# Performance work log

Measured on AMD Instinct MI355X. Metric: run time of the kernel, lower is better.

## Reference

```python
import jax, jax.numpy as jnp
import numpy as np

B, S, E = 16, 1024, 512
D = 2 * E            # dim of concatenated embeddings, input to QKV and MLP
H1, H2 = 2048, 1024  # hidden_dims
SCALE = float(1.0 / np.sqrt(E))  # code scales by embedding_dim**0.5 (the init arg, not D)


def setup_inputs() -> dict:
    key = jax.random.key(0)
    k = jax.random.split(key, 12)

    def lin_w(kk, fan_in, fan_out):
        return jax.random.normal(kk, (fan_in, fan_out), jnp.float32) * float(1.0 / np.sqrt(fan_in))

    return {
        "emb1": jax.random.normal(k[0], (B, S, E), jnp.float32),
        "emb2": jax.random.normal(k[1], (B, S, E), jnp.float32),
        # query-row masks; all ones (a 0 would -inf an entire softmax row -> NaN)
        "mask1": jnp.ones((B, S // 2), jnp.int32),
        "mask2": jnp.ones((B, S // 2), jnp.int32),
        "Wq": lin_w(k[2], D, D), "bq": jnp.zeros((D,), jnp.float32),
        "Wk": lin_w(k[3], D, D), "bk": jnp.zeros((D,), jnp.float32),
        "Wv": lin_w(k[4], D, D), "bv": jnp.zeros((D,), jnp.float32),
        "W1": lin_w(k[5], D, H1), "b1": jnp.zeros((H1,), jnp.float32),
        "W2": lin_w(k[6], H1, H2), "b2": jnp.zeros((H2,), jnp.float32),
        "W3": lin_w(k[7], H2, 1), "b3": jnp.zeros((1,), jnp.float32),
    }


def reference(emb1, emb2, mask1, mask2, Wq, bq, Wk, bk, Wv, bv, W1, b1, W2, b2, W3, b3):
    x = jnp.concatenate([emb1, emb2], axis=-1)        # [B, S, D]
    mask = jnp.concatenate([mask1, mask2], axis=-1)   # [B, S] (query-row mask)

    # QKV self-attention with query-only mask
    Q = x @ Wq + bq
    K = x @ Wk + bk
    V = x @ Wv + bv
    scores = jnp.einsum("bqd,bkd->bqk", Q, K) * SCALE  # [B, S, S]
    scores = jnp.where(mask[:, :, None] == 0, -jnp.inf, scores)
    attn = jax.nn.softmax(scores, axis=-1)
    attended = jnp.einsum("bqk,bkd->bqd", attn, V)     # [B, S, D]

    # MLP head (Dropout is identity in eval mode)
    h = jax.nn.relu(attended @ W1 + b1)
    h = jax.nn.relu(h @ W2 + b2)
    logits = h @ W3 + b3                               # [B, S, 1]
    return jax.nn.sigmoid(logits)
```

## Files before the change

### kernel.cpp

```cpp
#include <hip/hip_runtime.h>
#include <math.h>

#define DEV __device__ __forceinline__
#define SB0() __builtin_amdgcn_sched_barrier(0)

typedef unsigned short u16;
typedef unsigned int   u32;
typedef __bf16 bf16x8 __attribute__((ext_vector_type(8)));
typedef float  f32x4  __attribute__((ext_vector_type(4)));
typedef u16    u16x8  __attribute__((ext_vector_type(8)));
typedef u16    u16x4  __attribute__((ext_vector_type(4)));

DEV u16 f2b(float f) {
  u32 u = __builtin_bit_cast(u32, f);
  u = (u + 0x7FFFu + ((u >> 16) & 1u)) >> 16;
  return (u16)u;
}
DEV float b2f(u16 h) { u32 u = (u32)h << 16; return __builtin_bit_cast(float, u); }

DEV void gl_lds16(const u16* g, u16* l) {
  __builtin_amdgcn_global_load_lds((const __attribute__((address_space(1))) void*)g,
                                   (__attribute__((address_space(3))) void*)l, 16, 0, 0);
}

DEV float wred_max(float v) {
#pragma unroll
  for (int o = 32; o > 0; o >>= 1) v = fmaxf(v, __shfl_xor(v, o, 64));
  return v;
}
DEV float wred_sum(float v) {
#pragma unroll
  for (int o = 32; o > 0; o >>= 1) v += __shfl_xor(v, o, 64);
  return v;
}

__global__ __launch_bounds__(256) void prep(
    const float* __restrict__ e1, const float* __restrict__ e2, u16* __restrict__ xb,
    const float* __restrict__ Wq, const float* __restrict__ Wk, const float* __restrict__ Wv,
    const float* __restrict__ W1, const float* __restrict__ W2,
    u16* __restrict__ WTQKV, u16* __restrict__ W1T, u16* __restrict__ W2T,
    const float* __restrict__ bq, const float* __restrict__ bk, float* __restrict__ bf) {
  __shared__ float tile[64][65];
  const int bid = blockIdx.x;
  if (bid < 8192) {
    const size_t idx = ((size_t)bid * 256 + threadIdx.x) * 8;
    const int d = (int)(idx & 1023);
    const size_t row = idx >> 10;
    const float* s = (d < 512) ? (e1 + row * 512 + d) : (e2 + row * 512 + (d - 512));
    f32x4 a = *(const f32x4*)s;
    f32x4 b = *(const f32x4*)(s + 4);
    u16x8 o;
    o[0]=f2b(a[0]); o[1]=f2b(a[1]); o[2]=f2b(a[2]); o[3]=f2b(a[3]);
    o[4]=f2b(b[0]); o[5]=f2b(b[1]); o[6]=f2b(b[2]); o[7]=f2b(b[3]);
    *(u16x8*)(xb + idx) = o;
    return;
  }
  if (bid >= 9984) {
    int i = (bid - 9984) * 256 + threadIdx.x;
    bf[i] = (i < 1024) ? bq[i] : bk[i - 1024];
    return;
  }
  const float* W; u16* WT; int ldi, ldo, bx, by;
  if (bid < 8448)      { W = Wq; WT = WTQKV;              ldi = 1024; ldo = 1024; int v = bid - 8192; bx = v & 15; by = v >> 4; }
  else if (bid < 8704) { W = Wk; WT = WTQKV + 1024*1024;  ldi = 1024; ldo = 1024; int v = bid - 8448; bx = v & 15; by = v >> 4; }
  else if (bid < 8960) { W = Wv; WT = WTQKV + 2048*1024;  ldi = 1024; ldo = 1024; int v = bid - 8704; bx = v & 15; by = v >> 4; }
  else if (bid < 9472) { W = W1; WT = W1T;                ldi = 2048; ldo = 1024; int v = bid - 8960; bx = v & 31; by = v >> 5; }
  else                 { W = W2; WT = W2T;                ldi = 1024; ldo = 2048; int v = bid - 9472; bx = v & 15; by = v >> 4; }
  const int tx = threadIdx.x & 63, ty = threadIdx.x >> 6;
  const int r0 = by * 64, c0 = bx * 64;
#pragma unroll
  for (int i = 0; i < 16; ++i)
    tile[ty + 4*i][tx] = W[(size_t)(r0 + ty + 4*i) * ldi + c0 + tx];
  __syncthreads();
#pragma unroll
  for (int i = 0; i < 16; ++i)
    WT[(size_t)(c0 + ty + 4*i) * ldo + r0 + tx] = f2b(tile[tx][ty + 4*i]);
}

template<int F32OUT, int RELU, int RBIAS>
__global__ __launch_bounds__(512, 2) void gemm256(
    const u16* __restrict__ A, int lda, long long sA,
    const u16* __restrict__ B, int ldb, long long sB,
    void* __restrict__ C, int ldc, long long sC,
    const float* __restrict__ bias, float scale, int K) {
  __shared__ __align__(16) u16 lds[2][2][16384];

  const int t  = threadIdx.x;
  const int ln = t & 63, wv = t >> 6;

  int bx, by, bz;
  {
    const int gx = gridDim.x, gy = gridDim.y, gz = gridDim.z;
    const int nwg = gx * gy * gz;
    const int F = (blockIdx.z * gy + blockIdx.y) * gx + blockIdx.x;
    const int q = nwg >> 3;
    const int L = (F & 7) * q + (F >> 3);
    if (gz > 1) {
      const int pb = gx * gy;
      bz = L / pb; const int r = L - bz * pb;
      by = r / gx; bx = r - by * gx;
    } else {
      bz = 0;
      const int sh = ((gy & 7) == 0) ? 8 : 4;
      const int sw = gx * sh;
      const int sy = L / sw; const int r = L - sy * sw;
      bx = r / sh; by = sy * sh + (r - bx * sh);
    }
  }
  const int m0 = by * 256, n0 = bx * 256;
  A += (size_t)bz * (size_t)sA; B += (size_t)bz * (size_t)sB;

  const int gl = (ln & 7) ^ (ln >> 3);
  const u16* gAs = A + (size_t)(m0 + (t >> 3)) * lda + gl * 8;
  const u16* gBs = B + (size_t)(n0 + (t >> 3)) * ldb + gl * 8;

  const int l15 = ln & 15, lhi = ln >> 4;
  const int wm = (wv >> 2) * 128, wn = (wv & 3) * 64;
  const int colk0 = ((lhi ^ (l15 & 7)) << 3);
  const int colk1 = (((4 + lhi) ^ (l15 & 7)) << 3);
  const int rcA = (wv >> 2) * 8192 + l15 * 64;
  const int rcB = ((wv & 3) >> 1) * 8192 + (wv & 1) * 4096 + l15 * 64;

  f32x4 acc[8][4] = {};
  bf16x8 Af[4][2], Bf[4][2];
  const int KT = K >> 6, NIT = KT >> 1;

#define STG(T, OP, H, LD, GS)                                              \
  if ((T) < KT) {                                                          \
    const u16* _s = (GS) + (size_t)(H) * 128 * (size_t)(LD) + (size_t)(T) * 64; \
    u16* _d = &lds[(T) & 1][OP][(H) * 8192 + wv * 512];                    \
    gl_lds16(_s, _d); gl_lds16(_s + 64 * (size_t)(LD), _d + 4096);         \
  }
#define RDA(BUF, ILO) {                                                    \
  _Pragma("unroll") for (int ii = 0; ii < 4; ++ii) {                       \
    Af[ii][0] = *(const bf16x8*)&lds[BUF][0][rcA + ((ILO) + ii) * 1024 + colk0]; \
    Af[ii][1] = *(const bf16x8*)&lds[BUF][0][rcA + ((ILO) + ii) * 1024 + colk1]; } }
#define RDB(BUF, JLO) {                                                    \
  _Pragma("unroll") for (int jj = 0; jj < 2; ++jj) {                       \
    Bf[(JLO) + jj][0] = *(const bf16x8*)&lds[BUF][1][rcB + ((JLO) + jj) * 1024 + colk0]; \
    Bf[(JLO) + jj][1] = *(const bf16x8*)&lds[BUF][1][rcB + ((JLO) + jj) * 1024 + colk1]; } }
#define MM(ILO, JLO) {                                                     \
  _Pragma("unroll") for (int ii = 0; ii < 4; ++ii)                         \
  _Pragma("unroll") for (int jj = 0; jj < 2; ++jj) {                       \
    acc[(ILO)+ii][(JLO)+jj] = __builtin_amdgcn_mfma_f32_16x16x32_bf16(Af[ii][0], Bf[(JLO)+jj][0], acc[(ILO)+ii][(JLO)+jj], 0, 0, 0); \
    acc[(ILO)+ii][(JLO)+jj] = __builtin_amdgcn_mfma_f32_16x16x32_bf16(Af[ii][1], Bf[(JLO)+jj][1], acc[(ILO)+ii][(JLO)+jj], 0, 0, 0); } }
#define BAR() __builtin_amdgcn_s_barrier()
#define PRIO(x) __builtin_amdgcn_s_setprio(x)

  STG(0, 0, 0, lda, gAs); STG(0, 0, 1, lda, gAs);
  STG(0, 1, 0, ldb, gBs); STG(0, 1, 1, ldb, gBs);
  STG(1, 1, 0, ldb, gBs); STG(1, 1, 1, ldb, gBs);
  asm volatile("s_waitcnt vmcnt(4)" ::: "memory");
  SB0(); BAR();

  for (int it = 0; it < NIT; ++it) {
    const int T0 = it << 1, T1 = T0 + 1;
    RDB(0, 0); RDA(0, 0); STG(T1, 0, 0, lda, gAs);
    BAR();
    PRIO(1); MM(0, 0); PRIO(0); BAR();
    RDB(0, 2); STG(T1, 0, 1, lda, gAs);
    BAR();
    PRIO(1); MM(0, 2); PRIO(0); BAR();
    RDA(0, 4); STG(T0 + 2, 1, 0, ldb, gBs);
    BAR();
    PRIO(1); MM(4, 0); PRIO(0); BAR();
    STG(T0 + 2, 1, 1, ldb, gBs);
    BAR();
    PRIO(1); MM(4, 2); PRIO(0);
    if (T0 + 2 < KT) { asm volatile("s_waitcnt vmcnt(4)" ::: "memory"); }
    else             { asm volatile("s_waitcnt vmcnt(0)" ::: "memory"); }
    SB0(); BAR();
    RDB(1, 0); RDA(1, 0); STG(T0 + 2, 0, 0, lda, gAs);
    BAR();
    PRIO(1); MM(0, 0); PRIO(0); BAR();
    RDB(1, 2); STG(T0 + 2, 0, 1, lda, gAs);
    BAR();
    PRIO(1); MM(0, 2); PRIO(0); BAR();
    RDA(1, 4); STG(T0 + 3, 1, 0, ldb, gBs);
    BAR();
    PRIO(1); MM(4, 0); PRIO(0); BAR();
    STG(T0 + 3, 1, 1, ldb, gBs);
    BAR();
    PRIO(1); MM(4, 2); PRIO(0);
    if (T0 + 3 < KT) { asm volatile("s_waitcnt vmcnt(4)" ::: "memory"); }
    SB0(); BAR();
  }
#undef STG
#undef RDA
#undef RDB
#undef MM
#undef BAR
#undef PRIO

  const size_t cb = (size_t)bz * (size_t)sC;
  if (F32OUT) {
#pragma unroll
    for (int i = 0; i < 8; ++i) {
      const int rg = m0 + wm + i * 16 + lhi * 4;
#pragma unroll
      for (int j = 0; j < 4; ++j) {
        const int cg = n0 + wn + j * 16 + l15;
        const float cbv = (!RBIAS && bias) ? bias[cg] : 0.f;
#pragma unroll
        for (int r = 0; r < 4; ++r) {
          float v = acc[i][j][r] * scale + (RBIAS ? bias[rg + r] : cbv);
          if (RELU) v = fmaxf(v, 0.f);
          ((float*)C)[cb + (size_t)(rg + r) * ldc + cg] = v;
        }
      }
    }
  } else {
    u16* ep = ((u16*)lds) + wv * 8192;
#pragma unroll
    for (int i = 0; i < 8; ++i) {
      const int rg = m0 + wm + i * 16 + lhi * 4;
#pragma unroll
      for (int j = 0; j < 4; ++j) {
        const int cg = n0 + wn + j * 16 + l15;
        const float cbv = (!RBIAS && bias) ? bias[cg] : 0.f;
#pragma unroll
        for (int r = 0; r < 4; ++r) {
          float v = acc[i][j][r] * scale + (RBIAS ? bias[rg + r] : cbv);
          if (RELU) v = fmaxf(v, 0.f);
          const int lrow = i * 16 + lhi * 4 + r;
          const int lcol = (j * 16 + l15) ^ (((lrow >> 2) & 7) << 3);
          ep[lrow * 64 + lcol] = f2b(v);
        }
      }
    }
    asm volatile("s_waitcnt lgkmcnt(0)" ::: "memory");
    SB0();
    const int l3 = ln >> 3, c0 = (ln & 7) * 8;
#pragma unroll
    for (int rep = 0; rep < 16; ++rep) {
      const int lr = rep * 8 + l3;
      const int cs = c0 ^ (((lr >> 2) & 7) << 3);
      u16x8 v = *(const u16x8*)&ep[lr * 64 + cs];
      *(u16x8*)((u16*)C + cb + (size_t)(m0 + wm + lr) * ldc + n0 + wn + c0) = v;
    }
  }
}

__global__ __launch_bounds__(256) void softmax_mask(
    const float* __restrict__ sc, const int* __restrict__ m1,
    const int* __restrict__ m2, u16* __restrict__ attn) {
  __shared__ float red[8];
  const int row = blockIdx.x;
  const int b = row >> 10, q = row & 1023;
  const int mk = (q < 512) ? m1[b * 512 + q] : m2[b * 512 + q - 512];
  f32x4 v = ((const f32x4*)(sc + (size_t)row * 1024))[threadIdx.x];
  if (mk == 0) { v[0] = v[1] = v[2] = v[3] = -INFINITY; }
  float mx = fmaxf(fmaxf(v[0], v[1]), fmaxf(v[2], v[3]));
  mx = wred_max(mx);
  const int ln = threadIdx.x & 63, wv = threadIdx.x >> 6;
  if (ln == 0) red[wv] = mx;
  __syncthreads();
  mx = fmaxf(fmaxf(red[0], red[1]), fmaxf(red[2], red[3]));
  float e0 = __expf(v[0] - mx), e1 = __expf(v[1] - mx);
  float e2 = __expf(v[2] - mx), e3 = __expf(v[3] - mx);
  float s = wred_sum(e0 + e1 + e2 + e3);
  if (ln == 0) red[4 + wv] = s;
  __syncthreads();
  const float inv = 1.f / (red[4] + red[5] + red[6] + red[7]);
  u16x4 o; o[0] = f2b(e0 * inv); o[1] = f2b(e1 * inv); o[2] = f2b(e2 * inv); o[3] = f2b(e3 * inv);
  *(u16x4*)(attn + (size_t)row * 1024 + threadIdx.x * 4) = o;
}

__global__ __launch_bounds__(256) void logits_sigmoid(
    const u16* __restrict__ h2, const float* __restrict__ W3,
    const float* __restrict__ b3, float* __restrict__ out) {
  const int wid = (blockIdx.x * 256 + threadIdx.x) >> 6;
  const int ln = threadIdx.x & 63;
  const u16* r = h2 + (size_t)wid * 1024 + ln * 16;
  u16x8 v0 = *(const u16x8*)r;
  u16x8 v1 = *(const u16x8*)(r + 8);
  const float* w = W3 + ln * 16;
  float s = 0.f;
#pragma unroll
  for (int i = 0; i < 8; ++i) s += b2f(v0[i]) * w[i];
#pragma unroll
  for (int i = 0; i < 8; ++i) s += b2f(v1[i]) * w[8 + i];
#pragma unroll
  for (int o = 32; o > 0; o >>= 1) s += __shfl_down(s, o, 64);
  if (ln == 0) out[wid] = 1.f / (1.f + __expf(-(s + b3[0])));
}

extern "C" void kernel_launch(void* const* d_in, const int* in_sizes, int n_in,
                              void* d_out, int out_size, void* d_ws, size_t ws_size,
                              hipStream_t stream) {
  (void)in_sizes; (void)n_in; (void)out_size; (void)ws_size;
  const float* emb1 = (const float*)d_in[0];
  const float* emb2 = (const float*)d_in[1];
  const int*   mask1 = (const int*)d_in[2];
  const int*   mask2 = (const int*)d_in[3];
  const float* Wq = (const float*)d_in[4];  const float* bq = (const float*)d_in[5];
  const float* Wk = (const float*)d_in[6];  const float* bk = (const float*)d_in[7];
  const float* Wv = (const float*)d_in[8];  const float* bv = (const float*)d_in[9];
  const float* W1 = (const float*)d_in[10]; const float* b1 = (const float*)d_in[11];
  const float* W2 = (const float*)d_in[12]; const float* b2 = (const float*)d_in[13];
  const float* W3 = (const float*)d_in[14]; const float* b3 = (const float*)d_in[15];

  char* ws = (char*)d_ws;
  u16*  XB    = (u16*)(ws + 0);
  u16*  QK    = (u16*)(ws + 33554432);
  u16*  VT    = (u16*)(ws + 100663296);
  float* SC   = (float*)(ws + 134217728);
  u16*  WTQKV = (u16*)(ws + 201326592);
  u16*  W1T   = (u16*)(ws + 207618048);
  u16*  W2T   = (u16*)(ws + 211812352);
  float* BF_  = (float*)(ws + 216006656);
  u16*  ATTN  = XB;
  u16*  ATT   = (u16*)(ws + 134217728);
  u16*  H1    = QK;
  u16*  H2    = VT;
  float* out  = (float*)d_out;

  const float SCALE = 0.04419417382415922f;

  prep<<<9992, 256, 0, stream>>>(emb1, emb2, XB, Wq, Wk, Wv, W1, W2,
                                 WTQKV, W1T, W2T, bq, bk, BF_);

  gemm256<0, 0, 0><<<dim3(8, 64, 1), 512, 0, stream>>>(
      XB, 1024, 0, WTQKV, 1024, 0, QK, 2048, 0, BF_, 1.f, 1024);
  gemm256<0, 0, 1><<<dim3(64, 4, 1), 512, 0, stream>>>(
      WTQKV + 2048 * 1024, 1024, 0, XB, 1024, 0, VT, 16384, 0, bv, 1.f, 1024);
  gemm256<1, 0, 0><<<dim3(4, 4, 16), 512, 0, stream>>>(
      QK, 2048, 2097152LL, QK + 1024, 2048, 2097152LL,
      SC, 1024, 1048576LL, nullptr, SCALE, 1024);
  softmax_mask<<<16384, 256, 0, stream>>>(SC, mask1, mask2, ATTN);
  gemm256<0, 0, 0><<<dim3(4, 4, 16), 512, 0, stream>>>(
      ATTN, 1024, 1048576LL, VT, 16384, 1024LL,
      ATT, 1024, 1048576LL, nullptr, 1.f, 1024);
  gemm256<0, 1, 0><<<dim3(8, 64, 1), 512, 0, stream>>>(
      ATT, 1024, 0, W1T, 1024, 0, H1, 2048, 0, b1, 1.f, 1024);
  gemm256<0, 1, 0><<<dim3(4, 64, 1), 512, 0, stream>>>(
      H1, 2048, 0, W2T, 2048, 0, H2, 1024, 0, b2, 1.f, 2048);
  logits_sigmoid<<<4096, 256, 0, stream>>>(H2, W3, b3, out);
}
```

Baseline: 362.7 us.

## Fuse softmax into score GEMM epilogue and MLP head into last GEMM

The score GEMM now writes unnormalised bf16 exp values, with the mask applied, directly to the attention buffer, and accumulates row sums atomically. The PV GEMM divides by those row sums in its epilogue. This removes the fp32 score matrix round trip and the separate softmax kernel. The final W2 GEMM folds relu and the W3 dot product into its epilogue with atomic adds, replacing the H2 write and the logits kernel with a tiny sigmoid kernel. Exp is taken without subtracting the row max, so it can overflow if score magnitudes grow. Atomic accumulation also makes the row-sum order nondeterministic.

```diff
diff --git a/kernel.cpp b/kernel.cpp
--- a/kernel.cpp
+++ b/kernel.cpp
@@ -21,17 +21,6 @@
 DEV void gl_lds16(const u16* g, u16* l) {
   __builtin_amdgcn_global_load_lds((const __attribute__((address_space(1))) void*)g,
                                    (__attribute__((address_space(3))) void*)l, 16, 0, 0);
-}
-
-DEV float wred_max(float v) {
-#pragma unroll
-  for (int o = 32; o > 0; o >>= 1) v = fmaxf(v, __shfl_xor(v, o, 64));
-  return v;
-}
-DEV float wred_sum(float v) {
-#pragma unroll
-  for (int o = 32; o > 0; o >>= 1) v += __shfl_xor(v, o, 64);
-  return v;
 }
 
 __global__ __launch_bounds__(256) void prep(
@@ -77,12 +66,14 @@
     WT[(size_t)(c0 + ty + 4*i) * ldo + r0 + tx] = f2b(tile[tx][ty + 4*i]);
 }
 
-template<int F32OUT, int RELU, int RBIAS>
+template<int MODE>
 __global__ __launch_bounds__(512, 2) void gemm256(
     const u16* __restrict__ A, int lda, long long sA,
     const u16* __restrict__ B, int ldb, long long sB,
     void* __restrict__ C, int ldc, long long sC,
-    const float* __restrict__ bias, float scale, int K) {
+    const float* __restrict__ bias, float scale, int K,
+    const int* __restrict__ mk1, const int* __restrict__ mk2,
+    float* __restrict__ rsw, const float* __restrict__ w3, float* __restrict__ lg) {
   __shared__ __align__(16) u16 lds[2][2][16384];
 
   const int t  = threadIdx.x;
@@ -193,96 +184,99 @@
 #undef PRIO
 
   const size_t cb = (size_t)bz * (size_t)sC;
-  if (F32OUT) {
+
+  if (MODE == 5) {
+    float w3v[4];
+#pragma unroll
+    for (int j = 0; j < 4; ++j) w3v[j] = w3[n0 + wn + j * 16 + l15];
 #pragma unroll
     for (int i = 0; i < 8; ++i) {
       const int rg = m0 + wm + i * 16 + lhi * 4;
 #pragma unroll
-      for (int j = 0; j < 4; ++j) {
-        const int cg = n0 + wn + j * 16 + l15;
-        const float cbv = (!RBIAS && bias) ? bias[cg] : 0.f;
-#pragma unroll
-        for (int r = 0; r < 4; ++r) {
-          float v = acc[i][j][r] * scale + (RBIAS ? bias[rg + r] : cbv);
-          if (RELU) v = fmaxf(v, 0.f);
-          ((float*)C)[cb + (size_t)(rg + r) * ldc + cg] = v;
+      for (int r = 0; r < 4; ++r) {
+        float s = 0.f;
+#pragma unroll
+        for (int j = 0; j < 4; ++j) {
+          float v = acc[i][j][r] + bias[n0 + wn + j * 16 + l15];
+          v = fmaxf(v, 0.f);
+          s += v * w3v[j];
         }
+        s += __shfl_xor(s, 1, 64); s += __shfl_xor(s, 2, 64);
+        s += __shfl_xor(s, 4, 64); s += __shfl_xor(s, 8, 64);
+        if (l15 == 0) atomicAdd(&lg[rg + r], s);
+      }
+    }
+    return;
+  }
+
+  u16* ep = ((u16*)lds) + wv * 8192;
+
+  if (MODE == 3) {
+#pragma unroll
+    for (int i = 0; i < 8; ++i) {
+#pragma unroll
+      for (int r = 0; r < 4; ++r) {
+        const int rr = m0 + wm + i * 16 + lhi * 4 + r;
+        const int mk = (rr < 512) ? mk1[bz * 512 + rr] : mk2[bz * 512 + rr - 512];
+        const int lrow = i * 16 + lhi * 4 + r;
+        float s = 0.f;
+#pragma unroll
+        for (int j = 0; j < 4; ++j) {
+          float e = (mk != 0) ? __expf(acc[i][j][r] * scale) : 0.f;
+          const u16 eb = f2b(e);
+          s += b2f(eb);
+          const int lcol = (j * 16 + l15) ^ (((lrow >> 2) & 7) << 3);
+          ep[lrow * 64 + lcol] = eb;
+        }
+        s += __shfl_xor(s, 1, 64); s += __shfl_xor(s, 2, 64);
+        s += __shfl_xor(s, 4, 64); s += __shfl_xor(s, 8, 64);
+        if (l15 == 0) atomicAdd(&rsw[(size_t)bz * 1024 + rr], s);
       }
     }
   } else {
-    u16* ep = ((u16*)lds) + wv * 8192;
 #pragma unroll
     for (int i = 0; i < 8; ++i) {
-      const int rg = m0 + wm + i * 16 + lhi * 4;
+      const int rl = wm + i * 16 + lhi * 4;
+      float rv[4];
+#pragma unroll
+      for (int r = 0; r < 4; ++r) {
+        if (MODE == 2)      rv[r] = bias[m0 + rl + r];
+        else if (MODE == 4) rv[r] = 1.f / rsw[(size_t)bz * 1024 + m0 + rl + r];
+        else                rv[r] = 0.f;
+      }
 #pragma unroll
       for (int j = 0; j < 4; ++j) {
-        const int cg = n0 + wn + j * 16 + l15;
-        const float cbv = (!RBIAS && bias) ? bias[cg] : 0.f;
+        const float cbv = (MODE == 0 || MODE == 1) ? bias[n0 + wn + j * 16 + l15] : 0.f;
 #pragma unroll
         for (int r = 0; r < 4; ++r) {
-          float v = acc[i][j][r] * scale + (RBIAS ? bias[rg + r] : cbv);
-          if (RELU) v = fmaxf(v, 0.f);
+          float v;
+          if (MODE == 4)      v = acc[i][j][r] * rv[r];
+          else if (MODE == 2) v = acc[i][j][r] + rv[r];
+          else                v = acc[i][j][r] + cbv;
+          if (MODE == 1) v = fmaxf(v, 0.f);
           const int lrow = i * 16 + lhi * 4 + r;
           const int lcol = (j * 16 + l15) ^ (((lrow >> 2) & 7) << 3);
           ep[lrow * 64 + lcol] = f2b(v);
         }
       }
     }
-    asm volatile("s_waitcnt lgkmcnt(0)" ::: "memory");
-    SB0();
-    const int l3 = ln >> 3, c0 = (ln & 7) * 8;
-#pragma unroll
-    for (int rep = 0; rep < 16; ++rep) {
-      const int lr = rep * 8 + l3;
-      const int cs = c0 ^ (((lr >> 2) & 7) << 3);
-      u16x8 v = *(const u16x8*)&ep[lr * 64 + cs];
-      *(u16x8*)((u16*)C + cb + (size_t)(m0 + wm + lr) * ldc + n0 + wn + c0) = v;
-    }
-  }
-}
-
-__global__ __launch_bounds__(256) void softmax_mask(
-    const float* __restrict__ sc, const int* __restrict__ m1,
-    const int* __restrict__ m2, u16* __restrict__ attn) {
-  __shared__ float red[8];
-  const int row = blockIdx.x;
-  const int b = row >> 10, q = row & 1023;
-  const int mk = (q < 512) ? m1[b * 512 + q] : m2[b * 512 + q - 512];
-  f32x4 v = ((const f32x4*)(sc + (size_t)row * 1024))[threadIdx.x];
-  if (mk == 0) { v[0] = v[1] = v[2] = v[3] = -INFINITY; }
-  float mx = fmaxf(fmaxf(v[0], v[1]), fmaxf(v[2], v[3]));
-  mx = wred_max(mx);
-  const int ln = threadIdx.x & 63, wv = threadIdx.x >> 6;
-  if (ln == 0) red[wv] = mx;
-  __syncthreads();
-  mx = fmaxf(fmaxf(red[0], red[1]), fmaxf(red[2], red[3]));
-  float e0 = __expf(v[0] - mx), e1 = __expf(v[1] - mx);
-  float e2 = __expf(v[2] - mx), e3 = __expf(v[3] - mx);
-  float s = wred_sum(e0 + e1 + e2 + e3);
-  if (ln == 0) red[4 + wv] = s;
-  __syncthreads();
-  const float inv = 1.f / (red[4] + red[5] + red[6] + red[7]);
-  u16x4 o; o[0] = f2b(e0 * inv); o[1] = f2b(e1 * inv); o[2] = f2b(e2 * inv); o[3] = f2b(e3 * inv);
-  *(u16x4*)(attn + (size_t)row * 1024 + threadIdx.x * 4) = o;
-}
-
-__global__ __launch_bounds__(256) void logits_sigmoid(
-    const u16* __restrict__ h2, const float* __restrict__ W3,
-    const float* __restrict__ b3, float* __restrict__ out) {
-  const int wid = (blockIdx.x * 256 + threadIdx.x) >> 6;
-  const int ln = threadIdx.x & 63;
-  const u16* r = h2 + (size_t)wid * 1024 + ln * 16;
-  u16x8 v0 = *(const u16x8*)r;
-  u16x8 v1 = *(const u16x8*)(r + 8);
-  const float* w = W3 + ln * 16;
-  float s = 0.f;
-#pragma unroll
-  for (int i = 0; i < 8; ++i) s += b2f(v0[i]) * w[i];
-#pragma unroll
-  for (int i = 0; i < 8; ++i) s += b2f(v1[i]) * w[8 + i];
-#pragma unroll
-  for (int o = 32; o > 0; o >>= 1) s += __shfl_down(s, o, 64);
-  if (ln == 0) out[wid] = 1.f / (1.f + __expf(-(s + b3[0])));
+  }
+  asm volatile("s_waitcnt lgkmcnt(0)" ::: "memory");
+  SB0();
+  const int l3 = ln >> 3, c0 = (ln & 7) * 8;
+#pragma unroll
+  for (int rep = 0; rep < 16; ++rep) {
+    const int lr = rep * 8 + l3;
+    const int cs = c0 ^ (((lr >> 2) & 7) << 3);
+    u16x8 v = *(const u16x8*)&ep[lr * 64 + cs];
+    *(u16x8*)((u16*)C + cb + (size_t)(m0 + wm + lr) * ldc + n0 + wn + c0) = v;
+  }
+}
+
+__global__ __launch_bounds__(256) void sigmoid_k(
+    const float* __restrict__ lg, const float* __restrict__ b3, float* __restrict__ out) {
+  const int i = blockIdx.x * 256 + threadIdx.x;
+  out[i] = 1.f / (1.f + __expf(-(lg[i] + b3[0])));
 }
 
 extern "C" void kernel_launch(void* const* d_in, const int* in_sizes, int n_in,
@@ -304,36 +298,43 @@
   u16*  XB    = (u16*)(ws + 0);
   u16*  QK    = (u16*)(ws + 33554432);
   u16*  VT    = (u16*)(ws + 100663296);
-  float* SC   = (float*)(ws + 134217728);
-  u16*  WTQKV = (u16*)(ws + 201326592);
-  u16*  W1T   = (u16*)(ws + 207618048);
-  u16*  W2T   = (u16*)(ws + 211812352);
-  float* BF_  = (float*)(ws + 216006656);
-  u16*  ATTN  = XB;
   u16*  ATT   = (u16*)(ws + 134217728);
+  u16*  WTQKV = (u16*)(ws + 167772160);
+  u16*  W1T   = (u16*)(ws + 174063616);
+  u16*  W2T   = (u16*)(ws + 178257920);
+  float* BF_  = (float*)(ws + 182452224);
+  float* RS   = (float*)(ws + 182460416);
+  float* LG   = (float*)(ws + 182525952);
+  u16*  E     = XB;
   u16*  H1    = QK;
-  u16*  H2    = VT;
   float* out  = (float*)d_out;
 
   const float SCALE = 0.04419417382415922f;
+
+  hipMemsetAsync(RS, 0, 131072, stream);
 
   prep<<<9992, 256, 0, stream>>>(emb1, emb2, XB, Wq, Wk, Wv, W1, W2,
                                  WTQKV, W1T, W2T, bq, bk, BF_);
 
-  gemm256<0, 0, 0><<<dim3(8, 64, 1), 512, 0, stream>>>(
-      XB, 1024, 0, WTQKV, 1024, 0, QK, 2048, 0, BF_, 1.f, 1024);
-  gemm256<0, 0, 1><<<dim3(64, 4, 1), 512, 0, stream>>>(
-      WTQKV + 2048 * 1024, 1024, 0, XB, 1024, 0, VT, 16384, 0, bv, 1.f, 1024);
-  gemm256<1, 0, 0><<<dim3(4, 4, 16), 512, 0, stream>>>(
+  gemm256<0><<<dim3(8, 64, 1), 512, 0, stream>>>(
+      XB, 1024, 0, WTQKV, 1024, 0, QK, 2048, 0, BF_, 1.f, 1024,
+      nullptr, nullptr, nullptr, nullptr, nullptr);
+  gemm256<2><<<dim3(64, 4, 1), 512, 0, stream>>>(
+      WTQKV + 2048 * 1024, 1024, 0, XB, 1024, 0, VT, 16384, 0, bv, 1.f, 1024,
+      nullptr, nullptr, nullptr, nullptr, nullptr);
+  gemm256<3><<<dim3(4, 4, 16), 512, 0, stream>>>(
       QK, 2048, 2097152LL, QK + 1024, 2048, 2097152LL,
-      SC, 1024, 1048576LL, nullptr, SCALE, 1024);
-  softmax_mask<<<16384, 256, 0, stream>>>(SC, mask1, mask2, ATTN);
-  gemm256<0, 0, 0><<<dim3(4, 4, 16), 512, 0, stream>>>(
-      ATTN, 1024, 1048576LL, VT, 16384, 1024LL,
-      ATT, 1024, 1048576LL, nullptr, 1.f, 1024);
-  gemm256<0, 1, 0><<<dim3(8, 64, 1), 512, 0, stream>>>(
-      ATT, 1024, 0, W1T, 1024, 0, H1, 2048, 0, b1, 1.f, 1024);
-  gemm256<0, 1, 0><<<dim3(4, 64, 1), 512, 0, stream>>>(
-      H1, 2048, 0, W2T, 2048, 0, H2, 1024, 0, b2, 1.f, 2048);
-  logits_sigmoid<<<4096, 256, 0, stream>>>(H2, W3, b3, out);
-}
+      E, 1024, 1048576LL, nullptr, SCALE, 1024,
+      mask1, mask2, RS, nullptr, nullptr);
+  gemm256<4><<<dim3(4, 4, 16), 512, 0, stream>>>(
+      E, 1024, 1048576LL, VT, 16384, 1024LL,
+      ATT, 1024, 1048576LL, nullptr, 1.f, 1024,
+      nullptr, nullptr, RS, nullptr, nullptr);
+  gemm256<1><<<dim3(8, 64, 1), 512, 0, stream>>>(
+      ATT, 1024, 0, W1T, 1024, 0, H1, 2048, 0, b1, 1.f, 1024,
+      nullptr, nullptr, nullptr, nullptr, nullptr);
+  gemm256<5><<<dim3(4, 64, 1), 512, 0, stream>>>(
+      H1, 2048, 0, W2T, 2048, 0, nullptr, 1024, 0, b2, 1.f, 2048,
+      nullptr, nullptr, nullptr, W3, LG);
+  sigmoid_k<<<64, 256, 0, stream>>>(LG, b3, out);
+}
```

After: 348.6 us. -3.9%, faster.
